# Kernel optimization log

Measured on AMD Instinct MI355X. Metric: run time of the kernel, lower is better.

## Reference

```python
import jax, jax.numpy as jnp
import numpy as np

# dims (see shape_source)
B, S, DM, H, CIN, COUT, E = 4, 1024, 256, 8, 23, 256, 16
D2 = 2 * DM                                  # MoE dim = cat(attn_out, queries)
HE = int(D2 * 4 * 2 / 3)                     # geglu/expert hidden = 1365
CAP = max(4, min(S, int(S * 2.0 / E)))       # eval capacity_factor=2.0 -> 128
THRESH = 0.2                                 # threshold_eval for 2nd expert
BAL_COEF, Z_COEF = 0.01, 0.001


def _gelu(x):
    return jax.nn.gelu(x, approximate=False)  # torch nn.GELU default = erf


def _layernorm(x, g, b, eps=1e-5):
    m = x.mean(-1, keepdims=True)
    v = ((x - m) ** 2).mean(-1, keepdims=True)
    return (x - m) * jax.lax.rsqrt(v + eps) * g + b


def _rmsnorm(x, g):
    # st-moe RMSNorm: F.normalize(x) * sqrt(d) * gamma
    n = jnp.sqrt((x * x).sum(-1, keepdims=True))
    return x / jnp.maximum(n, 1e-12) * jnp.float32(np.sqrt(x.shape[-1])) * g


def _geglu_ff(x, g, w1, b1, mult, w2, b2):
    # st-moe Expert with prenorm=True: RMSNorm -> Linear -> GEGLU -> Linear
    h = _rmsnorm(x, g) @ w1 + b1
    a, gate = jnp.split(h, 2, axis=-1)
    return (_gelu(gate) * a * mult) @ w2 + b2


def _mha(q_in, k_in, v_in, wq, bq, wk, bk, wv, bv, wo, bo):
    b, sq, d = q_in.shape
    hd = d // H
    def heads(t):
        return t.reshape(b, -1, H, hd).transpose(0, 2, 1, 3)  # (b,H,s,hd)
    q = heads(q_in @ wq + bq)
    k = heads(k_in @ wk + bk)
    v = heads(v_in @ wv + bv)
    scale = jnp.float32(1.0 / np.sqrt(hd))
    att = jax.nn.softmax(jnp.einsum('bhqd,bhkd->bhqk', q, k) * scale, axis=-1)
    o = jnp.einsum('bhqk,bhkd->bhqd', att, v).transpose(0, 2, 1, 3).reshape(b, sq, d)
    return o @ wo + bo


def _moe(x, gate_w, ln_g, ln_b, w1, b1, w2, b2):
    # top-2 gating with threshold + capacity, dense dispatch/combine (eval semantics)
    logits = jnp.einsum('bnd,ed->bne', x, gate_w)
    raw = jax.nn.softmax(logits, axis=-1)
    gates2, idx2 = jax.lax.top_k(raw, 2)                       # (b,n,2)
    gates2 = gates2 / jnp.maximum(gates2.sum(-1, keepdims=True), 1e-9)
    g1, g2 = gates2[..., 0], gates2[..., 1]
    route2 = (g2 > THRESH).astype(x.dtype)
    oh1 = jax.nn.one_hot(idx2[..., 0], E, dtype=x.dtype)       # (b,n,e)
    oh2 = jax.nn.one_hot(idx2[..., 1], E, dtype=x.dtype) * route2[..., None]
    pos1 = jnp.cumsum(oh1, axis=1) - oh1                       # slot within expert
    pos2 = jnp.cumsum(oh2, axis=1) - oh2 + oh1.sum(axis=1, keepdims=True)
    keep1 = oh1 * (pos1 < CAP).astype(x.dtype)
    keep2 = oh2 * (pos2 < CAP).astype(x.dtype)
    capoh1 = jax.nn.one_hot(jnp.clip(pos1, 0, CAP - 1).astype(jnp.int32), CAP, dtype=x.dtype)
    capoh2 = jax.nn.one_hot(jnp.clip(pos2, 0, CAP - 1).astype(jnp.int32), CAP, dtype=x.dtype)
    combine = (g1[..., None, None] * keep1[..., None] * capoh1
               + g2[..., None, None] * keep2[..., None] * capoh2)  # (b,n,e,c)
    dispatch = (combine > 0).astype(x.dtype)
    xin = jnp.einsum('bnec,bnd->ebcd', dispatch, x)            # (e,b,c,d)
    # Expert_alt: LayerNorm -> Linear -> LeakyReLU -> Linear, vectorized over experts
    h = _layernorm(xin, ln_g[:, None, None, :], ln_b[:, None, None, :])
    h = jax.nn.leaky_relu(jnp.einsum('ebcd,edh->ebch', h, w1) + b1[:, None, None, :])
    h = jnp.einsum('ebch,ehd->ebcd', h, w2) + b2[:, None, None, :]
    out = jnp.einsum('bnec,ebcd->bnd', combine, h)
    balance = (raw.mean(axis=1) * oh1.mean(axis=1)).mean() * jnp.float32(E * E) * BAL_COEF
    z = (jax.nn.logsumexp(logits, axis=-1) ** 2).mean() * Z_COEF
    return out, balance + z, balance, z


def setup_inputs() -> dict:
    key = jax.random.key(0)
    ks = iter(jax.random.split(key, 64))
    f32 = jnp.float32
    def rn(shape, std=0.02):
        return jax.random.normal(next(ks), shape, dtype=f32) * std
    return {
        'K': jax.random.normal(next(ks), (B, S, 3), dtype=f32),
        'V': jax.random.normal(next(ks), (B, S, CIN), dtype=f32),
        'Q': jax.random.normal(next(ks), (B, S, 3), dtype=f32),
        'w_topo': rn((3, DM)), 'b_topo': jnp.zeros((DM,), f32),
        'w_val': rn((CIN, DM)), 'b_val': jnp.zeros((DM,), f32),
        'wq': rn((DM, DM)), 'bq': jnp.zeros((DM,), f32),
        'wk': rn((DM, DM)), 'bk': jnp.zeros((DM,), f32),
        'wv': rn((DM, DM)), 'bv': jnp.zeros((DM,), f32),
        'wo': rn((DM, DM)), 'bo': jnp.zeros((DM,), f32),
        'ffb_g': jnp.ones((D2,), f32), 'ffb_w1': rn((D2, 2 * HE)),
        'ffb_b1': jnp.zeros((2 * HE,), f32), 'ffb_mult': jnp.ones((HE,), f32),
        'ffb_w2': rn((HE, D2)), 'ffb_b2': jnp.zeros((D2,), f32),
        'prenorm_g': jnp.ones((D2,), f32),
        'gate_w': rn((E, D2)),
        'exp_ln_g': jnp.ones((E, D2), f32), 'exp_ln_b': jnp.zeros((E, D2), f32),
        'exp_w1': rn((E, D2, HE)), 'exp_b1': jnp.zeros((E, HE), f32),
        'exp_w2': rn((E, HE, D2)), 'exp_b2': jnp.zeros((E, D2), f32),
        'ffa_g': jnp.ones((D2,), f32), 'ffa_w1': rn((D2, 2 * HE)),
        'ffa_b1': jnp.zeros((2 * HE,), f32), 'ffa_mult': jnp.ones((HE,), f32),
        'ffa_w2': rn((HE, D2)), 'ffa_b2': jnp.zeros((D2,), f32),
        'w_out': rn((D2, COUT)), 'b_out': jnp.zeros((COUT,), f32),
    }


def reference(K, V, Q, w_topo, b_topo, w_val, b_val, wq, bq, wk, bk, wv, bv, wo, bo,
              ffb_g, ffb_w1, ffb_b1, ffb_mult, ffb_w2, ffb_b2, prenorm_g, gate_w,
              exp_ln_g, exp_ln_b, exp_w1, exp_b1, exp_w2, exp_b2,
              ffa_g, ffa_w1, ffa_b1, ffa_mult, ffa_w2, ffa_b2, w_out, b_out):
    sk = K.shape[1]
    topo = _gelu(jnp.concatenate([K, Q], axis=1) @ w_topo + b_topo)
    keys, queries = topo[:, :sk], topo[:, sk:]
    values = _gelu(V @ w_val + b_val)
    attn = _mha(queries, keys, values, wq, bq, wk, bk, wv, bv, wo, bo)
    x = jnp.concatenate([attn, queries], axis=-1)      # (B, S, D2)
    # SparseMoEBlock with add_ff_before/add_ff_after = True (STMoE_prenorm)
    x = _geglu_ff(x, ffb_g, ffb_w1, ffb_b1, ffb_mult, ffb_w2, ffb_b2) + x
    moe_out, total_aux, bal, z = _moe(_rmsnorm(x, prenorm_g), gate_w,
                                      exp_ln_g, exp_ln_b, exp_w1, exp_b1, exp_w2, exp_b2)
    x = moe_out + x
    x = _geglu_ff(x, ffa_g, ffa_w1, ffa_b1, ffa_mult, ffa_w2, ffa_b2) + x
    out = _gelu(x @ w_out + b_out)
    return out, total_aux, bal, z
```

## Files before the change

kernel.cpp:

```cpp
#include <hip/hip_runtime.h>
#include <hip/hip_bf16.h>
#include <math.h>

#define CAPN 128

typedef short short8 __attribute__((ext_vector_type(8)));
typedef short short4v __attribute__((ext_vector_type(4)));
typedef float f32x4 __attribute__((ext_vector_type(4)));

__device__ __forceinline__ float gelu_f(float x){
  return 0.5f*x*(1.0f+erff(x*0.7071067811865476f));
}
__device__ __forceinline__ void split2(float v, __hip_bfloat16& h, __hip_bfloat16& l){
  h = __float2bfloat16(v);
  l = __float2bfloat16(v - __bfloat162float(h));
}
__device__ __forceinline__ void split2s(float v, short& h, short& l){
  __hip_bfloat16 hh = __float2bfloat16(v);
  __hip_bfloat16 ll = __float2bfloat16(v - __bfloat162float(hh));
  h = *(short*)&hh; l = *(short*)&ll;
}

__global__ __launch_bounds__(256) void topo_kernel(
    const float* __restrict__ K, const float* __restrict__ Q,
    const float* __restrict__ w, const float* __restrict__ b,
    __hip_bfloat16* __restrict__ khi, __hip_bfloat16* __restrict__ klo,
    __hip_bfloat16* __restrict__ qhi, __hip_bfloat16* __restrict__ qlo,
    float* __restrict__ qf32)
{
  int idx = blockIdx.x*256 + threadIdx.x;
  int d = idx & 255;
  int r = idx >> 8;
  int bb = r >> 11;
  int n  = r & 2047;
  const float* src = (n < 1024) ? (K + ((bb<<10) + n)*3)
                                : (Q + ((bb<<10) + (n-1024))*3);
  float v = b[d] + src[0]*w[d] + src[1]*w[256+d] + src[2]*w[512+d];
  v = gelu_f(v);
  int off = (((bb<<10) + (n & 1023))<<8) + d;
  __hip_bfloat16 h, l; split2(v, h, l);
  if (n < 1024){ khi[off] = h; klo[off] = l; }
  else         { qhi[off] = h; qlo[off] = l; qf32[off] = v; }
}

__global__ __launch_bounds__(256) void values_kernel(
    const float* __restrict__ V, const float* __restrict__ w,
    const float* __restrict__ b,
    __hip_bfloat16* __restrict__ vhi, __hip_bfloat16* __restrict__ vlo)
{
  int idx = blockIdx.x*256 + threadIdx.x;
  int d = idx & 255; int r = idx >> 8;
  const float* src = V + r*23;
  float acc = b[d];
  #pragma unroll
  for (int c=0;c<23;c++) acc += src[c]*w[c*256+d];
  acc = gelu_f(acc);
  __hip_bfloat16 h, l; split2(acc, h, l);
  vhi[idx] = h; vlo[idx] = l;
}

#define SLP 40
__global__ __launch_bounds__(256) void sgemm_kernel(
    const __hip_bfloat16* __restrict__ Ah_, const __hip_bfloat16* __restrict__ Al_,
    int lda, long sA,
    const __hip_bfloat16* __restrict__ Wh_, const __hip_bfloat16* __restrict__ Wl_,
    int ldw, long sW,
    const float* __restrict__ bias, int nbias, int bsplit, int bsplitPad, long sB,
    const float* __restrict__ R, int ldr,
    float* __restrict__ C, int ldc, long sC,
    int K, int act)
{
  int z = blockIdx.z;
  const short* Ah = (const short*)Ah_ + (long)z*sA;
  const short* Al = (const short*)Al_ + (long)z*sA;
  const short* Wh = (const short*)Wh_ + (long)z*sW;
  const short* Wl = (const short*)Wl_ + (long)z*sW;
  int bm = blockIdx.y*128, bn = blockIdx.x*128;
  int tid = threadIdx.x, lane = tid & 63, wave = tid >> 6;
  int wm = (wave & 1)*64, wn = (wave >> 1)*64;

  __shared__ short AsH[128*SLP], AsL[128*SLP], BsH[128*SLP], BsL[128*SLP];

  f32x4 acc[4][4];
  f32x4 zero4 = {0.f,0.f,0.f,0.f};
  #pragma unroll
  for (int i=0;i<4;i++)
    #pragma unroll
    for (int j=0;j<4;j++) acc[i][j] = zero4;

  int srow = tid >> 1, scol = (tid & 1)*16;
  int ml = lane & 15, q = lane >> 4;
  long abase = (long)(bm+srow)*lda + scol;
  long bbase = (long)(bn+srow)*ldw + scol;

  short8 ah0 = *(const short8*)&Ah[abase];
  short8 ah1 = *(const short8*)&Ah[abase + 8];
  short8 al0 = *(const short8*)&Al[abase];
  short8 al1 = *(const short8*)&Al[abase + 8];
  short8 bh0 = *(const short8*)&Wh[bbase];
  short8 bh1 = *(const short8*)&Wh[bbase + 8];
  short8 bl0 = *(const short8*)&Wl[bbase];
  short8 bl1 = *(const short8*)&Wl[bbase + 8];

  for (int k0 = 0; k0 < K; k0 += 32){
    __syncthreads();
    *(short8*)&AsH[srow*SLP + scol]     = ah0;
    *(short8*)&AsH[srow*SLP + scol + 8] = ah1;
    *(short8*)&AsL[srow*SLP + scol]     = al0;
    *(short8*)&AsL[srow*SLP + scol + 8] = al1;
    *(short8*)&BsH[srow*SLP + scol]     = bh0;
    *(short8*)&BsH[srow*SLP + scol + 8] = bh1;
    *(short8*)&BsL[srow*SLP + scol]     = bl0;
    *(short8*)&BsL[srow*SLP + scol + 8] = bl1;
    __syncthreads();
    if (k0 + 32 < K){
      long ab = abase + k0 + 32;
      long bb2 = bbase + k0 + 32;
      ah0 = *(const short8*)&Ah[ab];
      ah1 = *(const short8*)&Ah[ab + 8];
      al0 = *(const short8*)&Al[ab];
      al1 = *(const short8*)&Al[ab + 8];
      bh0 = *(const short8*)&Wh[bb2];
      bh1 = *(const short8*)&Wh[bb2 + 8];
      bl0 = *(const short8*)&Wl[bb2];
      bl1 = *(const short8*)&Wl[bb2 + 8];
    }
    short8 afh[4], afl[4], bfh[4], bfl[4];
    #pragma unroll
    for (int i=0;i<4;i++){
      afh[i] = *(const short8*)&AsH[(wm + 16*i + ml)*SLP + q*8];
      afl[i] = *(const short8*)&AsL[(wm + 16*i + ml)*SLP + q*8];
    }
    #pragma unroll
    for (int j=0;j<4;j++){
      bfh[j] = *(const short8*)&BsH[(wn + 16*j + ml)*SLP + q*8];
      bfl[j] = *(const short8*)&BsL[(wn + 16*j + ml)*SLP + q*8];
    }
    #pragma unroll
    for (int i=0;i<4;i++)
      #pragma unroll
      for (int j=0;j<4;j++){
        acc[i][j] = __builtin_amdgcn_mfma_f32_16x16x32_bf16(afh[i], bfh[j], acc[i][j], 0,0,0);
        acc[i][j] = __builtin_amdgcn_mfma_f32_16x16x32_bf16(afh[i], bfl[j], acc[i][j], 0,0,0);
        acc[i][j] = __builtin_amdgcn_mfma_f32_16x16x32_bf16(afl[i], bfh[j], acc[i][j], 0,0,0);
      }
  }

  const float* biasz = bias ? bias + (long)z*sB : nullptr;
  long coff = (long)z*sC;
  #pragma unroll
  for (int i=0;i<4;i++){
    #pragma unroll
    for (int r=0;r<4;r++){
      int gm = bm + wm + 16*i + q*4 + r;
      #pragma unroll
      for (int j=0;j<4;j++){
        int gn = bn + wn + 16*j + ml;
        float v = acc[i][j][r];
        if (biasz){
          int bi;
          if (bsplit){
            if (gn < bsplit) bi = gn;
            else if (gn >= bsplitPad && gn < bsplitPad + (nbias - bsplit)) bi = gn - (bsplitPad - bsplit);
            else bi = -1;
          } else bi = (gn < nbias) ? gn : -1;
          if (bi >= 0) v += biasz[bi];
        }
        if (act == 1) v = gelu_f(v);
        if (R) v += R[(long)gm*ldr + gn];
        C[coff + (long)gm*ldc + gn] = v;
      }
    }
  }
}

#define LP 56
__global__ __launch_bounds__(256) void bgemm_kernel(
    const __hip_bfloat16* __restrict__ A, int lda, long sA,
    const __hip_bfloat16* __restrict__ WT, int ldw, long sW,
    const float* __restrict__ bias, int nbias, int bsplit, int bsplitPad, long sB,
    const float* __restrict__ R, int ldr, long sR,
    void* __restrict__ C, int ldc, long sC, int cIsBf16,
    int K, int act)
{
  int z = blockIdx.z;
  const short* Ab = (const short*)A + (long)z*sA;
  const short* Bb = (const short*)WT + (long)z*sW;
  int bm = blockIdx.y*128, bn = blockIdx.x*128;
  int tid = threadIdx.x, lane = tid & 63, wave = tid >> 6;
  int wm = (wave & 1)*64, wn = (wave >> 1)*64;

  __shared__ short As[128*LP];
  __shared__ short Bs[128*LP];

  f32x4 acc[4][4];
  f32x4 zero4 = {0.f,0.f,0.f,0.f};
  #pragma unroll
  for (int i=0;i<4;i++)
    #pragma unroll
    for (int j=0;j<4;j++) acc[i][j] = zero4;

  int g0 = tid, g1 = tid + 256;
  int r0 = g0 >> 2, c0 = (g0 & 3) * 8;
  int r1 = g1 >> 2, c1 = (g1 & 3) * 8;
  int ml = lane & 15, q = lane >> 4;
  long a0base = (long)(bm+r0)*lda + c0;
  long a1base = (long)(bm+r1)*lda + c1;
  long b0base = (long)(bn+r0)*ldw + c0;
  long b1base = (long)(bn+r1)*ldw + c1;

  short8 av0 = *(const short8*)&Ab[a0base];
  short8 av1 = *(const short8*)&Ab[a1base];
  short8 bv0 = *(const short8*)&Bb[b0base];
  short8 bv1 = *(const short8*)&Bb[b1base];

  for (int k0 = 0; k0 < K; k0 += 32){
    __syncthreads();
    *(short8*)&As[r0*LP + c0] = av0;
    *(short8*)&As[r1*LP + c1] = av1;
    *(short8*)&Bs[r0*LP + c0] = bv0;
    *(short8*)&Bs[r1*LP + c1] = bv1;
    __syncthreads();
    if (k0 + 32 < K){
      av0 = *(const short8*)&Ab[a0base + k0 + 32];
      av1 = *(const short8*)&Ab[a1base + k0 + 32];
      bv0 = *(const short8*)&Bb[b0base + k0 + 32];
      bv1 = *(const short8*)&Bb[b1base + k0 + 32];
    }
    short8 af[4], bfv[4];
    #pragma unroll
    for (int i=0;i<4;i++) af[i]  = *(const short8*)&As[(wm + 16*i + ml)*LP + q*8];
    #pragma unroll
    for (int j=0;j<4;j++) bfv[j] = *(const short8*)&Bs[(wn + 16*j + ml)*LP + q*8];
    #pragma unroll
    for (int i=0;i<4;i++)
      #pragma unroll
      for (int j=0;j<4;j++)
        acc[i][j] = __builtin_amdgcn_mfma_f32_16x16x32_bf16(af[i], bfv[j], acc[i][j], 0,0,0);
  }

  const float* biasz = bias ? bias + (long)z*sB : nullptr;
  const float* Rz = R ? R + (long)z*sR : nullptr;
  long coff = (long)z*sC;
  #pragma unroll
  for (int i=0;i<4;i++){
    #pragma unroll
    for (int r=0;r<4;r++){
      int gm = bm + wm + 16*i + q*4 + r;
      #pragma unroll
      for (int j=0;j<4;j++){
        int gn = bn + wn + 16*j + ml;
        float v = acc[i][j][r];
        if (biasz){
          int bi;
          if (bsplit){
            if (gn < bsplit) bi = gn;
            else if (gn >= bsplitPad && gn < bsplitPad + (nbias - bsplit)) bi = gn - (bsplitPad - bsplit);
            else bi = -1;
          } else bi = (gn < nbias) ? gn : -1;
          if (bi >= 0) v += biasz[bi];
        }
        if (act == 2) v = (v > 0.f) ? v : 0.01f*v;
        if (Rz) v += Rz[(long)gm*ldr + gn];
        if (cIsBf16) ((__hip_bfloat16*)C)[coff + (long)gm*ldc + gn] = __float2bfloat16(v);
        else         ((float*)C)[coff + (long)gm*ldc + gn] = v;
      }
    }
  }
}

__global__ __launch_bounds__(256) void convT_kernel(
    const float* __restrict__ W, int N, int K, long sW,
    __hip_bfloat16* __restrict__ out, int Npad, int Kpad, long sO,
    int split, int splitPad)
{
  int z = blockIdx.z;
  int n0 = blockIdx.x*64, k0 = blockIdx.y*64;
  int tid = threadIdx.x;
  __shared__ float lds[64][65];
  #pragma unroll
  for (int i=0;i<16;i++){
    int e = tid + i*256;
    int kl = e >> 6, c = e & 63;
    int np = n0 + c;
    int ns;
    if (split){
      if (np < split) ns = np;
      else if (np >= splitPad && np < splitPad + (N - split)) ns = np - (splitPad - split);
      else ns = -1;
    } else ns = (np < N) ? np : -1;
    int k = k0 + kl;
    float v = (ns >= 0 && k < K) ? W[(long)z*sW + (long)k*N + ns] : 0.f;
    lds[kl][c] = v;
  }
  __syncthreads();
  #pragma unroll
  for (int i=0;i<16;i++){
    int e = tid + i*256;
    int nl = e >> 6, kl = e & 63;
    out[(long)z*sO + (long)(n0+nl)*Kpad + k0 + kl] = __float2bfloat16(lds[kl][nl]);
  }
}

__global__ __launch_bounds__(256) void convT2_kernel(
    const float* __restrict__ W, int N, int K,
    __hip_bfloat16* __restrict__ outh, __hip_bfloat16* __restrict__ outl,
    int Npad, int Kpad, int split, int splitPad)
{
  int n0 = blockIdx.x*64, k0 = blockIdx.y*64;
  int tid = threadIdx.x;
  __shared__ float lds[64][65];
  #pragma unroll
  for (int i=0;i<16;i++){
    int e = tid + i*256;
    int kl = e >> 6, c = e & 63;
    int np = n0 + c;
    int ns;
    if (split){
      if (np < split) ns = np;
      else if (np >= splitPad && np < splitPad + (N - split)) ns = np - (splitPad - split);
      else ns = -1;
    } else ns = (np < N) ? np : -1;
    int k = k0 + kl;
    float v = (ns >= 0 && k < K) ? W[(long)k*N + ns] : 0.f;
    lds[kl][c] = v;
  }
  __syncthreads();
  #pragma unroll
  for (int i=0;i<16;i++){
    int e = tid + i*256;
    int nl = e >> 6, kl = e & 63;
    float v = lds[kl][nl];
    __hip_bfloat16 h, l; split2(v, h, l);
    long o = (long)(n0+nl)*Kpad + k0 + kl;
    outh[o] = h; outl[o] = l;
  }
}

__global__ void pack_bias_kernel(const float* bq, const float* bk, const float* bv, float* out){
  int i = blockIdx.x*256 + threadIdx.x;
  if (i < 256) out[i] = bq[i];
  else if (i < 512) out[i] = bk[i-256];
  else if (i < 768) out[i] = bv[i-512];
}

__global__ __launch_bounds__(256) void qksplit_kernel(
    const float* __restrict__ QP,
    __hip_bfloat16* __restrict__ qsh, __hip_bfloat16* __restrict__ qsl,
    __hip_bfloat16* __restrict__ ksh, __hip_bfloat16* __restrict__ ksl)
{
  int idx = blockIdx.x*256 + threadIdx.x;
  float qv = QP[idx] * 0.17677669529663687f;
  __hip_bfloat16 h, l;
  split2(qv, h, l); qsh[idx] = h; qsl[idx] = l;
  float kv = QP[1048576 + idx];
  split2(kv, h, l); ksh[idx] = h; ksl[idx] = l;
}

__global__ __launch_bounds__(256) void vtrans_kernel(
    const float* __restrict__ VP,
    __hip_bfloat16* __restrict__ vth, __hip_bfloat16* __restrict__ vtl)
{
  int bh = blockIdx.y, bb = bh >> 3, h = bh & 7;
  int s0 = blockIdx.x*64;
  int tid = threadIdx.x;
  __shared__ float t[64][33];
  #pragma unroll
  for (int p=0;p<8;p++){
    int sl = (tid>>5) + p*8;
    int d = tid & 31;
    t[sl][d] = VP[((bb<<10)+s0+sl)*256 + h*32 + d];
  }
  __syncthreads();
  #pragma unroll
  for (int p=0;p<8;p++){
    int dl = (tid>>6) + p*4;
    int s = tid & 63;
    float v = t[s][dl];
    __hip_bfloat16 hh, ll; split2(v, hh, ll);
    vth[(bh*32+dl)*1024 + s0 + s] = hh;
    vtl[(bh*32+dl)*1024 + s0 + s] = ll;
  }
}

#define KSP 40
__global__ __launch_bounds__(256) void attn_mfma_kernel(
    const __hip_bfloat16* __restrict__ qsh_, const __hip_bfloat16* __restrict__ qsl_,
    const __hip_bfloat16* __restrict__ ksh_, const __hip_bfloat16* __restrict__ ksl_,
    const __hip_bfloat16* __restrict__ vth_, const __hip_bfloat16* __restrict__ vtl_,
    __hip_bfloat16* __restrict__ aoh, __hip_bfloat16* __restrict__ aol)
{
  const short* qsh = (const short*)qsh_; const short* qsl = (const short*)qsl_;
  const short* ksh = (const short*)ksh_; const short* ksl = (const short*)ksl_;
  const short* vth = (const short*)vth_; const short* vtl = (const short*)vtl_;
  int bh = blockIdx.y, bb = bh >> 3, h = bh & 7;
  int tid = threadIdx.x, lane = tid & 63, wave = tid >> 6;
  int ml = lane & 15, quad = lane >> 4;
  int q0 = blockIdx.x*64 + wave*16;

  __shared__ short KhS[32*KSP], KlS[32*KSP], VhS[32*KSP], VlS[32*KSP];
  __shared__ short PhS[4][16*KSP], PlS[4][16*KSP];
  short* Phw = PhS[wave]; short* Plw = PlS[wave];

  int qrow = (bb<<10) + q0 + ml;
  short8 qfh = *(const short8*)&qsh[qrow*256 + h*32 + quad*8];
  short8 qfl = *(const short8*)&qsl[qrow*256 + h*32 + quad*8];

  f32x4 O0 = {0.f,0.f,0.f,0.f}, O1 = {0.f,0.f,0.f,0.f};
  float m_[4], l_[4];
  #pragma unroll
  for (int r=0;r<4;r++){ m_[r] = -INFINITY; l_[r] = 0.f; }

  int sr = tid >> 3, sc = (tid & 7)*4;
  for (int k0 = 0; k0 < 1024; k0 += 32){
    int krow = (bb<<10) + k0 + sr;
    short4v kvh = *(const short4v*)&ksh[krow*256 + h*32 + sc];
    short4v kvl = *(const short4v*)&ksl[krow*256 + h*32 + sc];
    short4v vvh = *(const short4v*)&vth[(bh*32+sr)*1024 + k0 + sc];
    short4v vvl = *(const short4v*)&vtl[(bh*32+sr)*1024 + k0 + sc];
    __syncthreads();
    *(short4v*)&KhS[sr*KSP + sc] = kvh;
    *(short4v*)&KlS[sr*KSP + sc] = kvl;
    *(short4v*)&VhS[sr*KSP + sc] = vvh;
    *(short4v*)&VlS[sr*KSP + sc] = vvl;
    __syncthreads();
    short8 kb0h = *(const short8*)&KhS[ml*KSP + quad*8];
    short8 kb0l = *(const short8*)&KlS[ml*KSP + quad*8];
    short8 kb1h = *(const short8*)&KhS[(16+ml)*KSP + quad*8];
    short8 kb1l = *(const short8*)&KlS[(16+ml)*KSP + quad*8];
    f32x4 S0 = {0.f,0.f,0.f,0.f}, S1 = {0.f,0.f,0.f,0.f};
    S0 = __builtin_amdgcn_mfma_f32_16x16x32_bf16(qfl, kb0h, S0, 0,0,0);
    S0 = __builtin_amdgcn_mfma_f32_16x16x32_bf16(qfh, kb0l, S0, 0,0,0);
    S0 = __builtin_amdgcn_mfma_f32_16x16x32_bf16(qfh, kb0h, S0, 0,0,0);
    S1 = __builtin_amdgcn_mfma_f32_16x16x32_bf16(qfl, kb1h, S1, 0,0,0);
    S1 = __builtin_amdgcn_mfma_f32_16x16x32_bf16(qfh, kb1l, S1, 0,0,0);
    S1 = __builtin_amdgcn_mfma_f32_16x16x32_bf16(qfh, kb1h, S1, 0,0,0);
    #pragma unroll
    for (int r=0;r<4;r++){
      float tm = fmaxf(S0[r], S1[r]);
      #pragma unroll
      for (int o=1;o<16;o<<=1) tm = fmaxf(tm, __shfl_xor(tm, o, 64));
      float nm = fmaxf(m_[r], tm);
      float alpha = expf(m_[r] - nm);
      float p0 = expf(S0[r] - nm);
      float p1 = expf(S1[r] - nm);
      float ps = p0 + p1;
      #pragma unroll
      for (int o=1;o<16;o<<=1) ps += __shfl_xor(ps, o, 64);
      l_[r] = l_[r]*alpha + ps;
      m_[r] = nm;
      O0[r] *= alpha; O1[r] *= alpha;
      short sh, sl2;
      split2s(p0, sh, sl2);
      Phw[(quad*4+r)*KSP + ml] = sh;  Plw[(quad*4+r)*KSP + ml] = sl2;
      split2s(p1, sh, sl2);
      Phw[(quad*4+r)*KSP + 16 + ml] = sh;  Plw[(quad*4+r)*KSP + 16 + ml] = sl2;
    }
    short8 pAh = *(const short8*)&Phw[ml*KSP + quad*8];
    short8 pAl = *(const short8*)&Plw[ml*KSP + quad*8];
    short8 vb0h = *(const short8*)&VhS[ml*KSP + quad*8];
    short8 vb0l = *(const short8*)&VlS[ml*KSP + quad*8];
    short8 vb1h = *(const short8*)&VhS[(16+ml)*KSP + quad*8];
    short8 vb1l = *(const short8*)&VlS[(16+ml)*KSP + quad*8];
    O0 = __builtin_amdgcn_mfma_f32_16x16x32_bf16(pAl, vb0h, O0, 0,0,0);
    O0 = __builtin_amdgcn_mfma_f32_16x16x32_bf16(pAh, vb0l, O0, 0,0,0);
    O0 = __builtin_amdgcn_mfma_f32_16x16x32_bf16(pAh, vb0h, O0, 0,0,0);
    O1 = __builtin_amdgcn_mfma_f32_16x16x32_bf16(pAl, vb1h, O1, 0,0,0);
    O1 = __builtin_amdgcn_mfma_f32_16x16x32_bf16(pAh, vb1l, O1, 0,0,0);
    O1 = __builtin_amdgcn_mfma_f32_16x16x32_bf16(pAh, vb1h, O1, 0,0,0);
  }
  #pragma unroll
  for (int r=0;r<4;r++){
    float inv = 1.f / l_[r];
    int row = (bb<<10) + q0 + quad*4 + r;
    __hip_bfloat16 hh, ll;
    split2(O0[r]*inv, hh, ll);
    aoh[row*256 + h*32 + ml] = hh;       aol[row*256 + h*32 + ml] = ll;
    split2(O1[r]*inv, hh, ll);
    aoh[row*256 + h*32 + 16 + ml] = hh;  aol[row*256 + h*32 + 16 + ml] = ll;
  }
}

__global__ __launch_bounds__(256) void concat_kernel(
    const float* __restrict__ queries, float* __restrict__ x)
{
  int idx = blockIdx.x*256 + threadIdx.x;
  int d = idx & 255; int r = idx >> 8;
  x[(r<<9) + 256 + d] = queries[idx];
}

__global__ __launch_bounds__(256) void rmsnorm_kernel(
    const float* __restrict__ x, const float* __restrict__ g, float* __restrict__ y)
{
  int r = blockIdx.x; int tid = threadIdx.x;
  float v0 = x[(r<<9) + tid];
  float v1 = x[(r<<9) + 256 + tid];
  float ss = v0*v0 + v1*v1;
  #pragma unroll
  for (int off=32; off>0; off>>=1) ss += __shfl_down(ss, off, 64);
  __shared__ float wsum[4];
  if ((tid & 63) == 0) wsum[tid>>6] = ss;
  __syncthreads();
  float tot = wsum[0]+wsum[1]+wsum[2]+wsum[3];
  float scale = 22.62741699796952f / fmaxf(sqrtf(tot), 1e-12f);
  y[(r<<9) + tid]       = v0*scale*g[tid];
  y[(r<<9) + 256 + tid] = v1*scale*g[256+tid];
}

__global__ __launch_bounds__(256) void rmsnorm_split_kernel(
    const float* __restrict__ x, const float* __restrict__ g,
    __hip_bfloat16* __restrict__ yh, __hip_bfloat16* __restrict__ yl)
{
  int r = blockIdx.x; int tid = threadIdx.x;
  float v0 = x[(r<<9) + tid];
  float v1 = x[(r<<9) + 256 + tid];
  float ss = v0*v0 + v1*v1;
  #pragma unroll
  for (int off=32; off>0; off>>=1) ss += __shfl_down(ss, off, 64);
  __shared__ float wsum[4];
  if ((tid & 63) == 0) wsum[tid>>6] = ss;
  __syncthreads();
  float tot = wsum[0]+wsum[1]+wsum[2]+wsum[3];
  float scale = 22.62741699796952f / fmaxf(sqrtf(tot), 1e-12f);
  float a = v0*scale*g[tid];
  float b = v1*scale*g[256+tid];
  __hip_bfloat16 h, l;
  split2(a, h, l); yh[(r<<9)+tid] = h;     yl[(r<<9)+tid] = l;
  split2(b, h, l); yh[(r<<9)+256+tid] = h; yl[(r<<9)+256+tid] = l;
}

__global__ __launch_bounds__(256) void rmsnorm_bf_kernel(
    const float* __restrict__ x, const float* __restrict__ g, __hip_bfloat16* __restrict__ y)
{
  int r = blockIdx.x; int tid = threadIdx.x;
  float v0 = x[(r<<9) + tid];
  float v1 = x[(r<<9) + 256 + tid];
  float ss = v0*v0 + v1*v1;
  #pragma unroll
  for (int off=32; off>0; off>>=1) ss += __shfl_down(ss, off, 64);
  __shared__ float wsum[4];
  if ((tid & 63) == 0) wsum[tid>>6] = ss;
  __syncthreads();
  float tot = wsum[0]+wsum[1]+wsum[2]+wsum[3];
  float scale = 22.62741699796952f / fmaxf(sqrtf(tot), 1e-12f);
  y[(r<<9) + tid]       = __float2bfloat16(v0*scale*g[tid]);
  y[(r<<9) + 256 + tid] = __float2bfloat16(v1*scale*g[256+tid]);
}

__global__ __launch_bounds__(256) void glu_split_kernel(
    const float* __restrict__ h, const float* __restrict__ mult,
    __hip_bfloat16* __restrict__ th, __hip_bfloat16* __restrict__ tl)
{
  int idx = blockIdx.x*256 + threadIdx.x;
  int r = idx / 1408; int j = idx - r*1408;
  float v = 0.f;
  if (j < 1365){
    float a  = h[(long)r*2816 + j];
    float gt = h[(long)r*2816 + 1408 + j];
    v = gelu_f(gt) * a * mult[j];
  }
  __hip_bfloat16 hh, ll; split2(v, hh, ll);
  th[idx] = hh; tl[idx] = ll;
}

__global__ __launch_bounds__(256) void glu_bf_kernel(
    const __hip_bfloat16* __restrict__ h, const float* __restrict__ mult,
    __hip_bfloat16* __restrict__ t)
{
  int idx = blockIdx.x*256 + threadIdx.x;
  int r = idx / 1408; int j = idx - r*1408;
  float v = 0.f;
  if (j < 1365){
    float a  = __bfloat162float(h[(long)r*2816 + j]);
    float gt = __bfloat162float(h[(long)r*2816 + 1408 + j]);
    v = gelu_f(gt) * a * mult[j];
  }
  t[idx] = __float2bfloat16(v);
}

__global__ __launch_bounds__(256) void split32_kernel(
    const float* __restrict__ x, __hip_bfloat16* __restrict__ h, __hip_bfloat16* __restrict__ l)
{
  int idx = blockIdx.x*256 + threadIdx.x;
  float v = x[idx];
  __hip_bfloat16 hh, ll; split2(v, hh, ll);
  h[idx] = hh; l[idx] = ll;
}

__global__ void moe_init_kernel(float* sum_raw, float* z_sum)
{
  int i = threadIdx.x;
  if (i < 64) sum_raw[i] = 0.f;
  if (i == 0) *z_sum = 0.f;
}

__global__ __launch_bounds__(256) void gating_kernel(
    const float* __restrict__ xn, const float* __restrict__ gate_w,
    int* __restrict__ idx1, int* __restrict__ idx2, int* __restrict__ route,
    float* __restrict__ gg1, float* __restrict__ gg2,
    float* __restrict__ sum_raw, float* __restrict__ z_sum)
{
  int t = blockIdx.x; int tid = threadIdx.x;
  __shared__ float xrow[512];
  xrow[tid]     = xn[(t<<9)+tid];
  xrow[256+tid] = xn[(t<<9)+256+tid];
  __syncthreads();
  int e = tid >> 4, l16 = tid & 15;
  float p = 0.f;
  for (int d=l16; d<512; d+=16) p += xrow[d]*gate_w[(e<<9)+d];
  __shared__ float part[16][17];
  part[e][l16] = p;
  __syncthreads();
  __shared__ float raw[16];
  if (tid < 16){
    float s = 0.f;
    #pragma unroll
    for (int i=0;i<16;i++) s += part[tid][i];
    raw[tid] = s;
  }
  __syncthreads();
  if (tid == 0){
    float mx = -1e30f;
    #pragma unroll
    for (int i=0;i<16;i++) mx = fmaxf(mx, raw[i]);
    float r[16]; float sum = 0.f;
    #pragma unroll
    for (int i=0;i<16;i++){ r[i] = expf(raw[i]-mx); sum += r[i]; }
    float lse = mx + logf(sum);
    atomicAdd(z_sum, lse*lse);
    float inv = 1.f/sum;
    #pragma unroll
    for (int i=0;i<16;i++){ r[i] *= inv; raw[i] = r[i]; }
    int i1 = -1; float b1 = -1.f;
    #pragma unroll
    for (int i=0;i<16;i++) if (r[i] > b1){ b1 = r[i]; i1 = i; }
    int i2 = -1; float b2 = -1.f;
    #pragma unroll
    for (int i=0;i<16;i++) if (i != i1 && r[i] > b2){ b2 = r[i]; i2 = i; }
    float s2 = fmaxf(b1 + b2, 1e-9f);
    float g1n = b1/s2, g2n = b2/s2;
    idx1[t] = i1; idx2[t] = i2;
    route[t] = (g2n > 0.2f) ? 1 : 0;
    gg1[t] = g1n; gg2[t] = g2n;
  }
  __syncthreads();
  int bb = t >> 10;
  if (tid < 16) atomicAdd(&sum_raw[(bb<<4)+tid], raw[tid]);
}

__global__ __launch_bounds__(256) void scan_kernel(
    const int* __restrict__ idx1, const int* __restrict__ idx2, const int* __restrict__ route,
    int* __restrict__ ts1, int* __restrict__ ts2, int* __restrict__ slot_token,
    int* __restrict__ count1)
{
  int bb = blockIdx.x >> 4;
  int e  = blockIdx.x & 15;
  int tid = threadIdx.x;
  int tbase = (bb<<10) + tid*4;
  int4 i1 = *(const int4*)&idx1[tbase];
  int4 i2 = *(const int4*)&idx2[tbase];
  int4 rt = *(const int4*)&route[tbase];
  int m1[4] = { i1.x==e, i1.y==e, i1.z==e, i1.w==e };
  int m2[4] = { i2.x==e, i2.y==e, i2.z==e, i2.w==e };
  int r4[4] = { rt.x, rt.y, rt.z, rt.w };
  int c1 = m1[0]+m1[1]+m1[2]+m1[3];
  int c2 = (m2[0]&&r4[0]) + (m2[1]&&r4[1]) + (m2[2]&&r4[2]) + (m2[3]&&r4[3]);
  __shared__ int s1[256], s2v[256];
  s1[tid] = c1; s2v[tid] = c2;
  __syncthreads();
  for (int off=1; off<256; off<<=1){
    int v1 = (tid>=off) ? s1[tid-off] : 0;
    int v2 = (tid>=off) ? s2v[tid-off] : 0;
    __syncthreads();
    s1[tid] += v1; s2v[tid] += v2;
    __syncthreads();
  }
  int tot1 = s1[255], tot2 = s2v[255];
  int p1 = s1[tid] - c1;
  int p2 = s2v[tid] - c2;
  if (tid == 0) count1[(bb<<4)+e] = tot1;
  int base = ((e<<2)+bb)*CAPN;
  #pragma unroll
  for (int i=0;i<4;i++){
    int t = tbase + i;
    if (m1[i]){
      if (p1 < CAPN){ ts1[t] = base+p1; slot_token[base+p1] = t; }
      else ts1[t] = -1;
      p1++;
    }
    if (m2[i]){
      if (r4[i]){
        int pos = tot1 + p2;
        if (pos < CAPN){ ts2[t] = base+pos; slot_token[base+pos] = t; }
        else ts2[t] = -1;
        p2++;
      } else ts2[t] = -1;
    }
  }
  int filled = min(CAPN, tot1 + tot2);
  if (tid < CAPN && tid >= filled) slot_token[base+tid] = -1;
}

__global__ __launch_bounds__(256) void gather_ln_kernel(
    const float* __restrict__ xn, const int* __restrict__ slot_token,
    const float* __restrict__ ln_g, const float* __restrict__ ln_b,
    __hip_bfloat16* __restrict__ xin)
{
  int s = blockIdx.x; int tid = threadIdx.x;
  int t = slot_token[s];
  int e = s >> 9;
  if (t < 0){
    xin[(s<<9)+tid] = __float2bfloat16(0.f);
    xin[(s<<9)+256+tid] = __float2bfloat16(0.f);
    return;
  }
  float v0 = xn[(t<<9)+tid];
  float v1 = xn[(t<<9)+256+tid];
  float sm = v0+v1, sq = v0*v0+v1*v1;
  #pragma unroll
  for (int off=32; off>0; off>>=1){
    sm += __shfl_down(sm, off, 64);
    sq += __shfl_down(sq, off, 64);
  }
  __shared__ float s1[4], s2buf[4];
  if ((tid & 63) == 0){ s1[tid>>6] = sm; s2buf[tid>>6] = sq; }
  __syncthreads();
  float tsm = s1[0]+s1[1]+s1[2]+s1[3];
  float tsq = s2buf[0]+s2buf[1]+s2buf[2]+s2buf[3];
  float mean = tsm * (1.f/512.f);
  float var = tsq * (1.f/512.f) - mean*mean;
  float rstd = rsqrtf(var + 1e-5f);
  xin[(s<<9)+tid]     = __float2bfloat16((v0-mean)*rstd*ln_g[(e<<9)+tid]     + ln_b[(e<<9)+tid]);
  xin[(s<<9)+256+tid] = __float2bfloat16((v1-mean)*rstd*ln_g[(e<<9)+256+tid] + ln_b[(e<<9)+256+tid]);
}

__global__ __launch_bounds__(256) void combine_kernel(
    float* __restrict__ x, const float* __restrict__ h2,
    const int* __restrict__ ts1, const int* __restrict__ ts2,
    const float* __restrict__ gg1, const float* __restrict__ gg2)
{
  int idx = blockIdx.x*256 + threadIdx.x;
  int t = idx >> 9; int d = idx & 511;
  float v = x[idx];
  int s1 = ts1[t]; if (s1 >= 0) v += gg1[t]*h2[(s1<<9)+d];
  int s2 = ts2[t]; if (s2 >= 0) v += gg2[t]*h2[(s2<<9)+d];
  x[idx] = v;
}

__global__ void aux_kernel(
    const float* __restrict__ sum_raw, const int* __restrict__ count1,
    const float* __restrict__ z_sum, float* __restrict__ out)
{
  int tid = threadIdx.x;
  float v = (sum_raw[tid] * (1.f/1024.f)) * ((float)count1[tid] * (1.f/1024.f));
  #pragma unroll
  for (int off=32; off>0; off>>=1) v += __shfl_down(v, off, 64);
  if (tid == 0){
    float bal = v * (1.f/64.f) * 256.f * 0.01f;
    float zl = (*z_sum) * (1.f/4096.f) * 0.001f;
    out[0] = bal + zl;
    out[1] = bal;
    out[2] = zl;
  }
}

extern "C" void kernel_launch(void* const* d_in, const int* in_sizes, int n_in,
                              void* d_out, int out_size, void* d_ws, size_t ws_size,
                              hipStream_t stream)
{
  const float* K_in   = (const float*)d_in[0];
  const float* V_in   = (const float*)d_in[1];
  const float* Q_in   = (const float*)d_in[2];
  const float* w_topo = (const float*)d_in[3];
  const float* b_topo = (const float*)d_in[4];
  const float* w_val  = (const float*)d_in[5];
  const float* b_val  = (const float*)d_in[6];
  const float* wq     = (const float*)d_in[7];
  const float* bq     = (const float*)d_in[8];
  const float* wk     = (const float*)d_in[9];
  const float* bk     = (const float*)d_in[10];
  const float* wv     = (const float*)d_in[11];
  const float* bv     = (const float*)d_in[12];
  const float* wo     = (const float*)d_in[13];
  const float* bo     = (const float*)d_in[14];
  const float* ffb_g  = (const float*)d_in[15];
  const float* ffb_w1 = (const float*)d_in[16];
  const float* ffb_b1 = (const float*)d_in[17];
  const float* ffb_mult=(const float*)d_in[18];
  const float* ffb_w2 = (const float*)d_in[19];
  const float* ffb_b2 = (const float*)d_in[20];
  const float* prenorm_g=(const float*)d_in[21];
  const float* gate_w = (const float*)d_in[22];
  const float* exp_ln_g=(const float*)d_in[23];
  const float* exp_ln_b=(const float*)d_in[24];
  const float* exp_w1 = (const float*)d_in[25];
  const float* exp_b1 = (const float*)d_in[26];
  const float* exp_w2 = (const float*)d_in[27];
  const float* exp_b2 = (const float*)d_in[28];
  const float* ffa_g  = (const float*)d_in[29];
  const float* ffa_w1 = (const float*)d_in[30];
  const float* ffa_b1 = (const float*)d_in[31];
  const float* ffa_mult=(const float*)d_in[32];
  const float* ffa_w2 = (const float*)d_in[33];
  const float* ffa_b2 = (const float*)d_in[34];
  const float* w_out  = (const float*)d_in[35];
  const float* b_out  = (const float*)d_in[36];
  float* dout = (float*)d_out;

  float* wsf = (float*)d_ws;
  int*   wsi = (int*)d_ws;

  const size_t A0 = 0;
  const size_t B0 = 11534336;
  const size_t OXA = 17301504;
  const size_t OXB = 19398656;
  const size_t OWP = 21495808;
  const size_t OMI = 21889024;

  __hip_bfloat16* qhi = (__hip_bfloat16*)(wsf + A0);
  __hip_bfloat16* khi = (__hip_bfloat16*)(wsf + A0 + 524288);
  __hip_bfloat16* vhi = (__hip_bfloat16*)(wsf + A0 + 1048576);
  __hip_bfloat16* qlo = (__hip_bfloat16*)(wsf + A0 + 1572864);
  __hip_bfloat16* klo = (__hip_bfloat16*)(wsf + A0 + 2097152);
  __hip_bfloat16* vlo = (__hip_bfloat16*)(wsf + A0 + 2621440);
  float* QP = wsf + A0 + 3145728;
  __hip_bfloat16* aohi = (__hip_bfloat16*)(wsf + A0 + 6291456);
  __hip_bfloat16* aolo = (__hip_bfloat16*)(wsf + A0 + 6815744);
  __hip_bfloat16* qsh = (__hip_bfloat16*)(wsf + A0);
  __hip_bfloat16* qsl = (__hip_bfloat16*)(wsf + A0 + 524288);
  __hip_bfloat16* ksh = (__hip_bfloat16*)(wsf + A0 + 1048576);
  __hip_bfloat16* ksl = (__hip_bfloat16*)(wsf + A0 + 1572864);
  __hip_bfloat16* vth = (__hip_bfloat16*)(wsf + A0 + 2097152);
  __hip_bfloat16* vtl = (__hip_bfloat16*)(wsf + A0 + 2621440);
  float* QF = wsf + B0 + 262144;
  float* Hb = wsf + A0;
  __hip_bfloat16* yh   = (__hip_bfloat16*)(wsf + B0);
  __hip_bfloat16* yl   = (__hip_bfloat16*)(wsf + B0 + 1048576);
  __hip_bfloat16* fw1h = (__hip_bfloat16*)(wsf + B0 + 2097152);
  __hip_bfloat16* fw1l = fw1h + 1441792;
  __hip_bfloat16* th   = (__hip_bfloat16*)(wsf + B0);
  __hip_bfloat16* tl   = (__hip_bfloat16*)(wsf + B0 + 2883584);
  __hip_bfloat16* fw2h = (__hip_bfloat16*)(wsf + A0);
  __hip_bfloat16* fw2l = fw2h + 720896;
  __hip_bfloat16* wte   = (__hip_bfloat16*)(wsf + A0);
  __hip_bfloat16* xin_bf= (__hip_bfloat16*)(wsf + A0 + 5767168);
  __hip_bfloat16* h1_bf = (__hip_bfloat16*)(wsf + A0 + 7864320);
  float* H2 = wsf + 13631488;
  float* YM = wsf + B0;
  __hip_bfloat16* y_bf = (__hip_bfloat16*)(wsf + A0);
  __hip_bfloat16* wf1  = (__hip_bfloat16*)(wsf + A0 + 1048576);
  __hip_bfloat16* h_bf = (__hip_bfloat16*)(wsf + A0 + 1769472);
  __hip_bfloat16* t_bf = (__hip_bfloat16*)(wsf + A0 + 7536640);
  __hip_bfloat16* wf2  = (__hip_bfloat16*)(wsf + A0 + 10420224);
  __hip_bfloat16* xah = (__hip_bfloat16*)(wsf + A0);
  __hip_bfloat16* xal = (__hip_bfloat16*)(wsf + A0 + 1048576);
  __hip_bfloat16* wp = (__hip_bfloat16*)(wsf + OWP);
  __hip_bfloat16* wqh = wp;            __hip_bfloat16* wkh = wp + 65536;
  __hip_bfloat16* wvh = wp + 131072;   __hip_bfloat16* wql = wp + 196608;
  __hip_bfloat16* wkl = wp + 262144;   __hip_bfloat16* wvl = wp + 327680;
  __hip_bfloat16* woh = wp + 393216;   __hip_bfloat16* wol = wp + 458752;
  __hip_bfloat16* wouth = wp + 524288; __hip_bfloat16* woutl = wp + 655360;

  int* idx1 = wsi + OMI + 0;
  int* idx2 = wsi + OMI + 4096;
  int* route= wsi + OMI + 8192;
  int* ts1  = wsi + OMI + 12288;
  int* ts2  = wsi + OMI + 16384;
  int* slot_token = wsi + OMI + 20480;
  int* count1     = wsi + OMI + 28672;
  float* sum_raw  = wsf + OMI + 28736;
  float* z_sum    = wsf + OMI + 28800;
  float* gg1      = wsf + OMI + 28864;
  float* gg2      = wsf + OMI + 32960;
  float* bias_qkv = wsf + OMI + 37056;

  convT2_kernel<<<dim3(4,4),  256, 0, stream>>>(wq, 256, 256, wqh, wql, 256, 256, 0, 0);
  convT2_kernel<<<dim3(4,4),  256, 0, stream>>>(wk, 256, 256, wkh, wkl, 256, 256, 0, 0);
  convT2_kernel<<<dim3(4,4),  256, 0, stream>>>(wv, 256, 256, wvh, wvl, 256, 256, 0, 0);
  convT2_kernel<<<dim3(4,4),  256, 0, stream>>>(wo, 256, 256, woh, wol, 256, 256, 0, 0);
  convT2_kernel<<<dim3(4,8),  256, 0, stream>>>(w_out, 256, 512, wouth, woutl, 256, 512, 0, 0);
  convT2_kernel<<<dim3(44,8), 256, 0, stream>>>(ffb_w1, 2730, 512, fw1h, fw1l, 2816, 512, 1365, 1408);
  pack_bias_kernel<<<3, 256, 0, stream>>>(bq, bk, bv, bias_qkv);

  topo_kernel<<<8192, 256, 0, stream>>>(K_in, Q_in, w_topo, b_topo, khi, klo, qhi, qlo, QF);
  values_kernel<<<4096, 256, 0, stream>>>(V_in, w_val, b_val, vhi, vlo);

  sgemm_kernel<<<dim3(2,32,3), 256, 0, stream>>>(
      qhi, qlo, 256, 1048576, wqh, wql, 256, 65536,
      bias_qkv, 256, 0, 0, 256, nullptr, 0, QP, 256, 1048576, 256, 0);

  qksplit_kernel<<<4096, 256, 0, stream>>>(QP, qsh, qsl, ksh, ksl);
  vtrans_kernel<<<dim3(16,32), 256, 0, stream>>>(QP + 2097152, vth, vtl);
  attn_mfma_kernel<<<dim3(16,32), 256, 0, stream>>>(qsh, qsl, ksh, ksl, vth, vtl, aohi, aolo);

  sgemm_kernel<<<dim3(2,32,1), 256, 0, stream>>>(
      aohi, aolo, 256, 0, woh, wol, 256, 0,
      bo, 256, 0, 0, 0, nullptr, 0, wsf+OXA, 512, 0, 256, 0);
  concat_kernel<<<4096, 256, 0, stream>>>(QF, wsf+OXA);

  rmsnorm_split_kernel<<<4096, 256, 0, stream>>>(wsf+OXA, ffb_g, yh, yl);
  sgemm_kernel<<<dim3(22,32,1), 256, 0, stream>>>(
      yh, yl, 512, 0, fw1h, fw1l, 512, 0,
      ffb_b1, 2730, 1365, 1408, 0, nullptr, 0, Hb, 2816, 0, 512, 0);
  glu_split_kernel<<<22528, 256, 0, stream>>>(Hb, ffb_mult, th, tl);
  convT2_kernel<<<dim3(8,22), 256, 0, stream>>>(ffb_w2, 512, 1365, fw2h, fw2l, 512, 1408, 0, 0);
  sgemm_kernel<<<dim3(4,32,1), 256, 0, stream>>>(
      th, tl, 1408, 0, fw2h, fw2l, 1408, 0,
      ffb_b2, 512, 0, 0, 0, wsf+OXA, 512, wsf+OXB, 512, 0, 1408, 0);

  rmsnorm_kernel<<<4096, 256, 0, stream>>>(wsf+OXB, prenorm_g, YM);
  moe_init_kernel<<<1, 64, 0, stream>>>(sum_raw, z_sum);
  gating_kernel<<<4096, 256, 0, stream>>>(YM, gate_w, idx1, idx2, route, gg1, gg2, sum_raw, z_sum);
  scan_kernel<<<64, 256, 0, stream>>>(idx1, idx2, route, ts1, ts2, slot_token, count1);
  gather_ln_kernel<<<8192, 256, 0, stream>>>(YM, slot_token, exp_ln_g, exp_ln_b, xin_bf);
  convT_kernel<<<dim3(22, 8, 16), 256, 0, stream>>>(exp_w1, 1365, 512, (long)512*1365,
                                                    wte, 1408, 512, (long)1408*512, 0, 0);
  bgemm_kernel<<<dim3(11,4,16), 256, 0, stream>>>(
      xin_bf, 512, (long)512*512, wte, 512, (long)1408*512,
      exp_b1, 1365, 0, 0, 1365, nullptr, 0, 0,
      h1_bf, 1408, (long)512*1408, 1, 512, 2);
  convT_kernel<<<dim3(8, 22, 16), 256, 0, stream>>>(exp_w2, 512, 1365, (long)1365*512,
                                                    wte, 512, 1408, (long)512*1408, 0, 0);
  bgemm_kernel<<<dim3(4,4,16), 256, 0, stream>>>(
      h1_bf, 1408, (long)512*1408, wte, 1408, (long)512*1408,
      exp_b2, 512, 0, 0, 512, nullptr, 0, 0,
      H2, 512, (long)512*512, 0, 1408, 0);
  combine_kernel<<<8192, 256, 0, stream>>>(wsf+OXB, H2, ts1, ts2, gg1, gg2);
  aux_kernel<<<1, 64, 0, stream>>>(sum_raw, count1, z_sum, dout + 4096*256);

  rmsnorm_bf_kernel<<<4096, 256, 0, stream>>>(wsf+OXB, ffa_g, y_bf);
  convT_kernel<<<dim3(44, 8, 1), 256, 0, stream>>>(ffa_w1, 2730, 512, 0,
                                                   wf1, 2816, 512, 0, 1365, 1408);
  bgemm_kernel<<<dim3(22,32,1), 256, 0, stream>>>(
      y_bf, 512, 0, wf1, 512, 0,
      ffa_b1, 2730, 1365, 1408, 0, nullptr, 0, 0,
      h_bf, 2816, 0, 1, 512, 0);
  glu_bf_kernel<<<22528, 256, 0, stream>>>(h_bf, ffa_mult, t_bf);
  convT_kernel<<<dim3(8, 22, 1), 256, 0, stream>>>(ffa_w2, 512, 1365, 0,
                                                   wf2, 512, 1408, 0, 0, 0);
  bgemm_kernel<<<dim3(4,32,1), 256, 0, stream>>>(
      t_bf, 1408, 0, wf2, 1408, 0,
      ffa_b2, 512, 0, 0, 0, wsf+OXB, 512, 0,
      wsf+OXA, 512, 0, 0, 1408, 0);

  split32_kernel<<<8192, 256, 0, stream>>>(wsf+OXA, xah, xal);
  sgemm_kernel<<<dim3(2,32,1), 256, 0, stream>>>(
      xah, xal, 512, 0, wouth, woutl, 512, 0,
      b_out, 256, 0, 0, 0, nullptr, 0, dout, 256, 0, 512, 1);
}
```

Before: 926.0 us.

## Add split-K to small-N GEMMs with separate reduction kernel

Adds split-K support to both GEMM kernels, writing fp32 partial tiles to a workspace, plus a reduce kernel that sums the partials and applies bias, activation and residual. It is used for the FF-before down-projection (4-way), FF-after down-projection (2-way) and output projection (4-way). These GEMMs launch only 64 to 128 blocks, which underfills the GPU, so the aim is more parallelism. The cost is extra global traffic for the partials and one extra launch per GEMM.

```diff
diff --git a/kernel.cpp b/kernel.cpp
--- a/kernel.cpp
+++ b/kernel.cpp
@@ -68,9 +68,11 @@
     const float* __restrict__ bias, int nbias, int bsplit, int bsplitPad, long sB,
     const float* __restrict__ R, int ldr,
     float* __restrict__ C, int ldc, long sC,
-    int K, int act)
-{
-  int z = blockIdx.z;
+    int K, int act,
+    float* __restrict__ P, long pz, int splitK)
+{
+  int z = blockIdx.z / splitK;
+  int kc = blockIdx.z - z*splitK;
   const short* Ah = (const short*)Ah_ + (long)z*sA;
   const short* Al = (const short*)Al_ + (long)z*sA;
   const short* Wh = (const short*)Wh_ + (long)z*sW;
@@ -93,16 +95,19 @@
   long abase = (long)(bm+srow)*lda + scol;
   long bbase = (long)(bn+srow)*ldw + scol;
 
-  short8 ah0 = *(const short8*)&Ah[abase];
-  short8 ah1 = *(const short8*)&Ah[abase + 8];
-  short8 al0 = *(const short8*)&Al[abase];
-  short8 al1 = *(const short8*)&Al[abase + 8];
-  short8 bh0 = *(const short8*)&Wh[bbase];
-  short8 bh1 = *(const short8*)&Wh[bbase + 8];
-  short8 bl0 = *(const short8*)&Wl[bbase];
-  short8 bl1 = *(const short8*)&Wl[bbase + 8];
-
-  for (int k0 = 0; k0 < K; k0 += 32){
+  int Kc = K / splitK;
+  int kbeg = kc * Kc, kend = kbeg + Kc;
+
+  short8 ah0 = *(const short8*)&Ah[abase + kbeg];
+  short8 ah1 = *(const short8*)&Ah[abase + kbeg + 8];
+  short8 al0 = *(const short8*)&Al[abase + kbeg];
+  short8 al1 = *(const short8*)&Al[abase + kbeg + 8];
+  short8 bh0 = *(const short8*)&Wh[bbase + kbeg];
+  short8 bh1 = *(const short8*)&Wh[bbase + kbeg + 8];
+  short8 bl0 = *(const short8*)&Wl[bbase + kbeg];
+  short8 bl1 = *(const short8*)&Wl[bbase + kbeg + 8];
+
+  for (int k0 = kbeg; k0 < kend; k0 += 32){
     __syncthreads();
     *(short8*)&AsH[srow*SLP + scol]     = ah0;
     *(short8*)&AsH[srow*SLP + scol + 8] = ah1;
@@ -113,7 +118,7 @@
     *(short8*)&BsL[srow*SLP + scol]     = bl0;
     *(short8*)&BsL[srow*SLP + scol + 8] = bl1;
     __syncthreads();
-    if (k0 + 32 < K){
+    if (k0 + 32 < kend){
       long ab = abase + k0 + 32;
       long bb2 = bbase + k0 + 32;
       ah0 = *(const short8*)&Ah[ab];
@@ -144,6 +149,22 @@
         acc[i][j] = __builtin_amdgcn_mfma_f32_16x16x32_bf16(afh[i], bfl[j], acc[i][j], 0,0,0);
         acc[i][j] = __builtin_amdgcn_mfma_f32_16x16x32_bf16(afl[i], bfh[j], acc[i][j], 0,0,0);
       }
+  }
+
+  if (P){
+    float* Pb = P + (long)blockIdx.z * pz;
+    #pragma unroll
+    for (int i=0;i<4;i++)
+      #pragma unroll
+      for (int r=0;r<4;r++){
+        int gm = bm + wm + 16*i + q*4 + r;
+        #pragma unroll
+        for (int j=0;j<4;j++){
+          int gn = bn + wn + 16*j + ml;
+          Pb[(long)gm*ldc + gn] = acc[i][j][r];
+        }
+      }
+    return;
   }
 
   const float* biasz = bias ? bias + (long)z*sB : nullptr;
@@ -181,9 +202,11 @@
     const float* __restrict__ bias, int nbias, int bsplit, int bsplitPad, long sB,
     const float* __restrict__ R, int ldr, long sR,
     void* __restrict__ C, int ldc, long sC, int cIsBf16,
-    int K, int act)
-{
-  int z = blockIdx.z;
+    int K, int act,
+    float* __restrict__ P, long pz, int splitK)
+{
+  int z = blockIdx.z / splitK;
+  int kc = blockIdx.z - z*splitK;
   const short* Ab = (const short*)A + (long)z*sA;
   const short* Bb = (const short*)WT + (long)z*sW;
   int bm = blockIdx.y*128, bn = blockIdx.x*128;
@@ -209,19 +232,22 @@
   long b0base = (long)(bn+r0)*ldw + c0;
   long b1base = (long)(bn+r1)*ldw + c1;
 
-  short8 av0 = *(const short8*)&Ab[a0base];
-  short8 av1 = *(const short8*)&Ab[a1base];
-  short8 bv0 = *(const short8*)&Bb[b0base];
-  short8 bv1 = *(const short8*)&Bb[b1base];
-
-  for (int k0 = 0; k0 < K; k0 += 32){
+  int Kc = K / splitK;
+  int kbeg = kc * Kc, kend = kbeg + Kc;
+
+  short8 av0 = *(const short8*)&Ab[a0base + kbeg];
+  short8 av1 = *(const short8*)&Ab[a1base + kbeg];
+  short8 bv0 = *(const short8*)&Bb[b0base + kbeg];
+  short8 bv1 = *(const short8*)&Bb[b1base + kbeg];
+
+  for (int k0 = kbeg; k0 < kend; k0 += 32){
     __syncthreads();
     *(short8*)&As[r0*LP + c0] = av0;
     *(short8*)&As[r1*LP + c1] = av1;
     *(short8*)&Bs[r0*LP + c0] = bv0;
     *(short8*)&Bs[r1*LP + c1] = bv1;
     __syncthreads();
-    if (k0 + 32 < K){
+    if (k0 + 32 < kend){
       av0 = *(const short8*)&Ab[a0base + k0 + 32];
       av1 = *(const short8*)&Ab[a1base + k0 + 32];
       bv0 = *(const short8*)&Bb[b0base + k0 + 32];
@@ -237,6 +263,22 @@
       #pragma unroll
       for (int j=0;j<4;j++)
         acc[i][j] = __builtin_amdgcn_mfma_f32_16x16x32_bf16(af[i], bfv[j], acc[i][j], 0,0,0);
+  }
+
+  if (P){
+    float* Pb = P + (long)blockIdx.z * pz;
+    #pragma unroll
+    for (int i=0;i<4;i++)
+      #pragma unroll
+      for (int r=0;r<4;r++){
+        int gm = bm + wm + 16*i + q*4 + r;
+        #pragma unroll
+        for (int j=0;j<4;j++){
+          int gn = bn + wn + 16*j + ml;
+          Pb[(long)gm*ldc + gn] = acc[i][j][r];
+        }
+      }
+    return;
   }
 
   const float* biasz = bias ? bias + (long)z*sB : nullptr;
@@ -267,6 +309,28 @@
       }
     }
   }
+}
+
+__global__ __launch_bounds__(256) void reduce_kernel(
+    const float* __restrict__ P, long zStride, int nsplit,
+    const float* __restrict__ bias,
+    const float* __restrict__ R, float* __restrict__ out,
+    int Nmask, int logN, int ldOut, int act, long total)
+{
+  long idx = (long)blockIdx.x*256 + threadIdx.x;
+  if (idx >= total) return;
+  long zz = idx / zStride;
+  long rem = idx - zz*zStride;
+  const float* Pb = P + zz*(long)nsplit*zStride + rem;
+  float v = 0.f;
+  for (int k=0;k<nsplit;k++) v += Pb[(long)k*zStride];
+  int n = (int)(idx & Nmask);
+  long row = idx >> logN;
+  if (bias) v += bias[n];
+  if (act == 1) v = gelu_f(v);
+  long o = row*(long)ldOut + n;
+  if (R) v += R[o];
+  out[o] = v;
 }
 
 __global__ __launch_bounds__(256) void convT_kernel(
@@ -842,6 +906,7 @@
   __hip_bfloat16* tl   = (__hip_bfloat16*)(wsf + B0 + 2883584);
   __hip_bfloat16* fw2h = (__hip_bfloat16*)(wsf + A0);
   __hip_bfloat16* fw2l = fw2h + 720896;
+  float* Pffb = wsf + A0 + 1048576;
   __hip_bfloat16* wte   = (__hip_bfloat16*)(wsf + A0);
   __hip_bfloat16* xin_bf= (__hip_bfloat16*)(wsf + A0 + 5767168);
   __hip_bfloat16* h1_bf = (__hip_bfloat16*)(wsf + A0 + 7864320);
@@ -852,8 +917,10 @@
   __hip_bfloat16* h_bf = (__hip_bfloat16*)(wsf + A0 + 1769472);
   __hip_bfloat16* t_bf = (__hip_bfloat16*)(wsf + A0 + 7536640);
   __hip_bfloat16* wf2  = (__hip_bfloat16*)(wsf + A0 + 10420224);
+  float* Pffa = wsf + B0;
   __hip_bfloat16* xah = (__hip_bfloat16*)(wsf + A0);
   __hip_bfloat16* xal = (__hip_bfloat16*)(wsf + A0 + 1048576);
+  float* Pout = wsf + A0 + 2097152;
   __hip_bfloat16* wp = (__hip_bfloat16*)(wsf + OWP);
   __hip_bfloat16* wqh = wp;            __hip_bfloat16* wkh = wp + 65536;
   __hip_bfloat16* wvh = wp + 131072;   __hip_bfloat16* wql = wp + 196608;
@@ -887,7 +954,8 @@
 
   sgemm_kernel<<<dim3(2,32,3), 256, 0, stream>>>(
       qhi, qlo, 256, 1048576, wqh, wql, 256, 65536,
-      bias_qkv, 256, 0, 0, 256, nullptr, 0, QP, 256, 1048576, 256, 0);
+      bias_qkv, 256, 0, 0, 256, nullptr, 0, QP, 256, 1048576, 256, 0,
+      nullptr, 0, 1);
 
   qksplit_kernel<<<4096, 256, 0, stream>>>(QP, qsh, qsl, ksh, ksl);
   vtrans_kernel<<<dim3(16,32), 256, 0, stream>>>(QP + 2097152, vth, vtl);
@@ -895,18 +963,23 @@
 
   sgemm_kernel<<<dim3(2,32,1), 256, 0, stream>>>(
       aohi, aolo, 256, 0, woh, wol, 256, 0,
-      bo, 256, 0, 0, 0, nullptr, 0, wsf+OXA, 512, 0, 256, 0);
+      bo, 256, 0, 0, 0, nullptr, 0, wsf+OXA, 512, 0, 256, 0,
+      nullptr, 0, 1);
   concat_kernel<<<4096, 256, 0, stream>>>(QF, wsf+OXA);
 
   rmsnorm_split_kernel<<<4096, 256, 0, stream>>>(wsf+OXA, ffb_g, yh, yl);
   sgemm_kernel<<<dim3(22,32,1), 256, 0, stream>>>(
       yh, yl, 512, 0, fw1h, fw1l, 512, 0,
-      ffb_b1, 2730, 1365, 1408, 0, nullptr, 0, Hb, 2816, 0, 512, 0);
+      ffb_b1, 2730, 1365, 1408, 0, nullptr, 0, Hb, 2816, 0, 512, 0,
+      nullptr, 0, 1);
   glu_split_kernel<<<22528, 256, 0, stream>>>(Hb, ffb_mult, th, tl);
   convT2_kernel<<<dim3(8,22), 256, 0, stream>>>(ffb_w2, 512, 1365, fw2h, fw2l, 512, 1408, 0, 0);
-  sgemm_kernel<<<dim3(4,32,1), 256, 0, stream>>>(
+  sgemm_kernel<<<dim3(4,32,4), 256, 0, stream>>>(
       th, tl, 1408, 0, fw2h, fw2l, 1408, 0,
-      ffb_b2, 512, 0, 0, 0, wsf+OXA, 512, wsf+OXB, 512, 0, 1408, 0);
+      nullptr, 0, 0, 0, 0, nullptr, 0, nullptr, 512, 0, 1408, 0,
+      Pffb, 2097152, 4);
+  reduce_kernel<<<8192, 256, 0, stream>>>(
+      Pffb, 2097152, 4, ffb_b2, wsf+OXA, wsf+OXB, 511, 9, 512, 0, 2097152);
 
   rmsnorm_kernel<<<4096, 256, 0, stream>>>(wsf+OXB, prenorm_g, YM);
   moe_init_kernel<<<1, 64, 0, stream>>>(sum_raw, z_sum);
@@ -918,13 +991,15 @@
   bgemm_kernel<<<dim3(11,4,16), 256, 0, stream>>>(
       xin_bf, 512, (long)512*512, wte, 512, (long)1408*512,
       exp_b1, 1365, 0, 0, 1365, nullptr, 0, 0,
-      h1_bf, 1408, (long)512*1408, 1, 512, 2);
+      h1_bf, 1408, (long)512*1408, 1, 512, 2,
+      nullptr, 0, 1);
   convT_kernel<<<dim3(8, 22, 16), 256, 0, stream>>>(exp_w2, 512, 1365, (long)1365*512,
                                                     wte, 512, 1408, (long)512*1408, 0, 0);
   bgemm_kernel<<<dim3(4,4,16), 256, 0, stream>>>(
       h1_bf, 1408, (long)512*1408, wte, 1408, (long)512*1408,
       exp_b2, 512, 0, 0, 512, nullptr, 0, 0,
-      H2, 512, (long)512*512, 0, 1408, 0);
+      H2, 512, (long)512*512, 0, 1408, 0,
+      nullptr, 0, 1);
   combine_kernel<<<8192, 256, 0, stream>>>(wsf+OXB, H2, ts1, ts2, gg1, gg2);
   aux_kernel<<<1, 64, 0, stream>>>(sum_raw, count1, z_sum, dout + 4096*256);
 
@@ -934,17 +1009,24 @@
   bgemm_kernel<<<dim3(22,32,1), 256, 0, stream>>>(
       y_bf, 512, 0, wf1, 512, 0,
       ffa_b1, 2730, 1365, 1408, 0, nullptr, 0, 0,
-      h_bf, 2816, 0, 1, 512, 0);
+      h_bf, 2816, 0, 1, 512, 0,
+      nullptr, 0, 1);
   glu_bf_kernel<<<22528, 256, 0, stream>>>(h_bf, ffa_mult, t_bf);
   convT_kernel<<<dim3(8, 22, 1), 256, 0, stream>>>(ffa_w2, 512, 1365, 0,
                                                    wf2, 512, 1408, 0, 0, 0);
-  bgemm_kernel<<<dim3(4,32,1), 256, 0, stream>>>(
+  bgemm_kernel<<<dim3(4,32,2), 256, 0, stream>>>(
       t_bf, 1408, 0, wf2, 1408, 0,
-      ffa_b2, 512, 0, 0, 0, wsf+OXB, 512, 0,
-      wsf+OXA, 512, 0, 0, 1408, 0);
+      nullptr, 0, 0, 0, 0, nullptr, 0, 0,
+      nullptr, 512, 0, 0, 1408, 0,
+      Pffa, 2097152, 2);
+  reduce_kernel<<<8192, 256, 0, stream>>>(
+      Pffa, 2097152, 2, ffa_b2, wsf+OXB, wsf+OXA, 511, 9, 512, 0, 2097152);
 
   split32_kernel<<<8192, 256, 0, stream>>>(wsf+OXA, xah, xal);
-  sgemm_kernel<<<dim3(2,32,1), 256, 0, stream>>>(
+  sgemm_kernel<<<dim3(2,32,4), 256, 0, stream>>>(
       xah, xal, 512, 0, wouth, woutl, 512, 0,
-      b_out, 256, 0, 0, 0, nullptr, 0, dout, 256, 0, 512, 1);
-}
+      nullptr, 0, 0, 0, 0, nullptr, 0, nullptr, 256, 0, 512, 0,
+      Pout, 1048576, 4);
+  reduce_kernel<<<4096, 256, 0, stream>>>(
+      Pout, 1048576, 4, b_out, nullptr, dout, 255, 8, 256, 1, 1048576);
+}
```

Measured after the change: 858.3 us. -7.3%, faster.
